# Optimization experiments

Measured on AMD Instinct MI355X. Metric: run time of the kernel, lower is better.

## Reference

```python
import jax, jax.numpy as jnp
import numpy as np
from jax import lax

B, N, CIN, COUT, FPS, K, TCH, M, H = 8, 4096, 128, 256, 1024, 24, 256, 32, 4
HD = TCH // H
BN_SCALE = 1.0 / np.sqrt(1.0 + 1e-5)  # eval-mode BN: running_mean=0, running_var=1


def _gather(points, idx):
    # points [B,N,C], idx [B,S] or [B,S,K] -> gathered points
    return jax.vmap(lambda p, i: p[i])(points, idx)


def _bn(x, g, b):
    return x * (g * BN_SCALE) + b


def _ln(x, g, b):
    mu = jnp.mean(x, -1, keepdims=True)
    v = jnp.var(x, -1, keepdims=True)
    return (x - mu) / jnp.sqrt(v + 1e-5) * g + b


def _gelu(x):
    return jax.nn.gelu(x, approximate=False)


def _fps(xyz, npoint, farthest0):
    Bb, Nn, _ = xyz.shape
    def step(carry, _):
        dmin, far = carry
        c = jax.vmap(lambda p, i: p[i])(xyz, far)  # [B,3]
        d = jnp.sum((xyz - c[:, None, :]) ** 2, -1)
        dmin = jnp.minimum(dmin, d)
        return (dmin, jnp.argmax(dmin, -1)), far
    init = (jnp.full((Bb, Nn), 1e10, xyz.dtype), farthest0)
    _, cents = lax.scan(step, init, None, length=npoint)
    return cents.T  # [B, npoint]


def _sqdist(src, dst):
    d = -2.0 * jnp.einsum('bnc,bmc->bnm', src, dst)
    d = d + jnp.sum(src ** 2, -1)[:, :, None]
    d = d + jnp.sum(dst ** 2, -1)[:, None, :]
    return d


def _forward(xyz, x, t, farthest0, Wproj, gproj, bproj, Wl1, gl1, bl1, Wl2, gl2, bl2,
             Wc1, gc1, bc1, Wc2, gc2, bc2, Wq, Wk, Wv, Wo,
             ln1g, ln1b, Wqkv, Wao, ln2g, ln2b, Wf1, Wf2):
    # --- GenerateGraph: FPS + KNN grouping ---
    fps_idx = _fps(xyz, FPS, farthest0)            # [B,S]
    new_xyz = _gather(xyz, fps_idx)                # [B,S,3]
    xT = jnp.transpose(x, (0, 2, 1))               # [B,N,Cin]
    new_pts = _gather(xT, fps_idx)                 # [B,S,Cin]
    dist = _sqdist(new_xyz, xyz)                   # [B,S,N]
    _, idx = lax.top_k(-dist, K)                   # [B,S,K] nearest neighbors
    grouped = _gather(xT, idx)                     # [B,S,K,Cin]
    edge = grouped - new_pts[:, :, None, :]
    # --- Local: Conv1DBR proj + Conv1DBRRes (channels-last, 1x1 convs = GEMM) ---
    h = _gelu(_bn(jnp.einsum('bskc,oc->bsko', edge, Wproj), gproj, bproj))
    r = _gelu(_bn(jnp.einsum('bsko,po->bskp', h, Wl1), gl1, bl1))
    r = _bn(jnp.einsum('bskp,op->bsko', r, Wl2), gl2, bl2)
    h = _gelu(r + h)
    f = jnp.max(h, axis=2)                         # adaptive_max_pool over k -> [B,S,O]
    # --- Channel (ca): Conv1DBRRes on centroid features ---
    r = _gelu(_bn(f @ Wc1.T, gc1, bc1))
    r = _bn(r @ Wc2.T, gc2, bc2)
    f = _gelu(r + f)
    x_out = jnp.transpose(f, (0, 2, 1))            # [B,O,S]
    # --- Local2Former: tokens attend to local features ---
    q = t @ Wq.T
    kk = f @ Wk.T
    v = f @ Wv.T
    a = jax.nn.softmax(jnp.einsum('bmd,bsd->bms', q, kk) * (TCH ** -0.5), axis=-1)
    t = t + jnp.einsum('bms,bsd->bmd', a, v) @ Wo.T
    # --- Former: one pre-norm encoder layer (MHA + MLP) ---
    hn = _ln(t, ln1g, ln1b)
    qkv = (hn @ Wqkv.T).reshape(B, M, 3, H, HD).transpose(2, 0, 3, 1, 4)
    qh, kh, vh = qkv[0], qkv[1], qkv[2]            # [B,H,M,hd]
    attn = jax.nn.softmax(jnp.einsum('bhmd,bhnd->bhmn', qh, kh) * (HD ** -0.5), axis=-1)
    o = jnp.einsum('bhmn,bhnd->bhmd', attn, vh).transpose(0, 2, 1, 3).reshape(B, M, TCH)
    t = t + o @ Wao.T
    hn = _ln(t, ln2g, ln2b)
    t = t + _gelu(hn @ Wf1.T) @ Wf2.T
    return new_xyz, x_out, t


def setup_inputs() -> dict:
    key = jax.random.key(0)
    ks = jax.random.split(key, 40)
    def w(k, o, i):
        return jax.random.normal(k, (o, i), jnp.float32) / np.sqrt(i)
    def g(k, c):
        return 1.0 + 0.1 * jax.random.normal(k, (c,), jnp.float32)
    def bta(k, c):
        return 0.1 * jax.random.normal(k, (c,), jnp.float32)
    inp = {
        'xyz': jax.random.normal(ks[0], (B, N, 3), jnp.float32),
        'x': jax.random.normal(ks[1], (B, CIN, N), jnp.float32),
        't': jax.random.normal(ks[2], (B, M, TCH), jnp.float32),
        'farthest0': jax.random.randint(ks[3], (B,), 0, N),
        'Wproj': w(ks[4], COUT, CIN), 'gproj': g(ks[5], COUT), 'bproj': bta(ks[6], COUT),
        'Wl1': w(ks[7], COUT, COUT), 'gl1': g(ks[8], COUT), 'bl1': bta(ks[9], COUT),
        'Wl2': w(ks[10], COUT, COUT), 'gl2': g(ks[11], COUT), 'bl2': bta(ks[12], COUT),
        'Wc1': w(ks[13], COUT, COUT), 'gc1': g(ks[14], COUT), 'bc1': bta(ks[15], COUT),
        'Wc2': w(ks[16], COUT, COUT), 'gc2': g(ks[17], COUT), 'bc2': bta(ks[18], COUT),
        'Wq': w(ks[19], TCH, TCH), 'Wk': w(ks[20], TCH, COUT), 'Wv': w(ks[21], TCH, COUT),
        'Wo': w(ks[22], TCH, TCH),
        'ln1g': g(ks[23], TCH), 'ln1b': bta(ks[24], TCH),
        'Wqkv': w(ks[25], 3 * TCH, TCH), 'Wao': w(ks[26], TCH, TCH),
        'ln2g': g(ks[27], TCH), 'ln2b': bta(ks[28], TCH),
        'Wf1': w(ks[29], 2 * TCH, TCH), 'Wf2': w(ks[30], TCH, 2 * TCH),
    }
    return inp


def reference(xyz, x, t, farthest0, Wproj, gproj, bproj, Wl1, gl1, bl1, Wl2, gl2, bl2,
              Wc1, gc1, bc1, Wc2, gc2, bc2, Wq, Wk, Wv, Wo,
              ln1g, ln1b, Wqkv, Wao, ln2g, ln2b, Wf1, Wf2):
    return _forward(xyz, x, t, farthest0, Wproj, gproj, bproj, Wl1, gl1, bl1, Wl2, gl2, bl2,
                    Wc1, gc1, bc1, Wc2, gc2, bc2, Wq, Wk, Wv, Wo,
                    ln1g, ln1b, Wqkv, Wao, ln2g, ln2b, Wf1, Wf2)
```

## Files before the change

### kernel.cpp

```cpp
#include <hip/hip_runtime.h>
#include <math.h>

#define Bc 8
#define Nc 4096
#define CINc 128
#define COUTc 256
#define Sc 1024
#define Kc 24
#define TCHc 256
#define Mc 32
#define Hc 4
#define HDc 64
#define MBAT (Sc*Kc)

#define BN_SCALE_F 0.9999950000374997f

typedef __attribute__((ext_vector_type(8))) short bf16x8;
typedef __attribute__((ext_vector_type(4))) float f32x4;

__device__ __forceinline__ float b2f(short s){
  unsigned int u = ((unsigned int)(unsigned short)s) << 16;
  union { unsigned int u; float f; } c; c.u = u; return c.f;
}
__device__ __forceinline__ short f2b(float f){
  union { unsigned int u; float f; } c; c.f = f;
  unsigned int u = c.u;
  unsigned int r = (u + 0x7fffu + ((u >> 16) & 1u)) >> 16;
  return (short)(r & 0xffffu);
}
__device__ __forceinline__ float gelu_f(float v){
  return 0.5f * v * (1.f + erff(v * 0.7071067811865475f));
}
__device__ __forceinline__ float rdval(const float* p){ return *p; }
__device__ __forceinline__ float rdval(const short* p){ return b2f(*p); }
__device__ __forceinline__ void wrval(float* p, float v){ *p = v; }
__device__ __forceinline__ void wrval(short* p, float v){ *p = f2b(v); }

__device__ __forceinline__ void gl_lds16(const short* g, short* l){
  __builtin_amdgcn_global_load_lds(
     (const __attribute__((address_space(1))) void*)g,
     (__attribute__((address_space(3))) void*)l, 16, 0, 0);
}

template<int CTRL>
__device__ __forceinline__ double dpp_max_f64(double v){
  long long x = __double_as_longlong(v);
  int lo = (int)(unsigned int)(x & 0xFFFFFFFFLL);
  int hi = (int)(unsigned int)((unsigned long long)x >> 32);
  int plo = __builtin_amdgcn_update_dpp(lo, lo, CTRL, 0xF, 0xF, false);
  int phi = __builtin_amdgcn_update_dpp(hi, hi, CTRL, 0xF, 0xF, false);
  double p = __longlong_as_double((long long)(((unsigned long long)(unsigned int)phi << 32)
                                              | (unsigned int)plo));
  return fmax(v, p);
}
template<int CTRL>
__device__ __forceinline__ float dpp_min_f32(float v){
  int x = __float_as_int(v);
  int p = __builtin_amdgcn_update_dpp(x, x, CTRL, 0xF, 0xF, false);
  return fminf(v, __int_as_float(p));
}
template<int CTRL>
__device__ __forceinline__ unsigned dpp_min_u32(unsigned v){
  int p = __builtin_amdgcn_update_dpp((int)v, (int)v, CTRL, 0xF, 0xF, false);
  unsigned pu = (unsigned)p;
  return v < pu ? v : pu;
}

#define PREP_FPS 8
#define PREP_TX 4096
#define PREP_CVT 64
#define PREP_DD 128
#define PREP_TOTAL (PREP_FPS+PREP_TX+PREP_CVT+PREP_DD)

__global__ __launch_bounds__(256) void prep_kernel(
    const float* __restrict__ xyz, const int* __restrict__ far0, int* __restrict__ fps_idx,
    const float* __restrict__ x, short* __restrict__ xT,
    const float* __restrict__ Wproj, const float* __restrict__ Wl1, const float* __restrict__ Wl2,
    const float* __restrict__ Wc1, const float* __restrict__ Wc2,
    const float* __restrict__ Wk, const float* __restrict__ Wv,
    const float* __restrict__ Wq, const float* __restrict__ Wo,
    const float* __restrict__ Wqkv, const float* __restrict__ Wao,
    const float* __restrict__ Wf1, const float* __restrict__ Wf2,
    const float* __restrict__ t_in,
    short* __restrict__ wbf, float* __restrict__ dd){
  __shared__ double smem[6176];
  int bid = blockIdx.x, tid = threadIdx.x;
  if(bid < PREP_FPS){
    int b = bid;
    float* sx = (float*)smem;
    float* sy = sx + Nc;
    float* sz = sy + Nc;
    double* pwave = smem + (Nc*12)/8;
    const float* xb = xyz + (size_t)b*Nc*3;
    for(int i=tid; i<Nc; i+=256){
      const float* p = xb + i*3;
      sx[i]=p[0]; sy[i]=p[1]; sz[i]=p[2];
    }
    __syncthreads();
    float px[16], py[16], pz[16], dmin[16];
    unsigned int lokey[16];
#pragma unroll
    for(int j=0;j<16;j++){
      int n = tid + 256*j;
      px[j]=sx[n]; py[j]=sy[n]; pz[j]=sz[n];
      dmin[j]=1e10f;
      lokey[j]=(unsigned int)((Nc-1) - n);
    }
    int winner = far0[b] & (Nc-1);
    int* out = fps_idx + b*Sc;
    for(int it=0; it<Sc; it++){
      if(tid==0) out[it] = winner;
      float cx=sx[winner], cy=sy[winner], cz=sz[winner];
      double key[16];
#pragma unroll
      for(int j=0;j<16;j++){
        float dx = __fsub_rn(px[j], cx);
        float dy = __fsub_rn(py[j], cy);
        float dz = __fsub_rn(pz[j], cz);
        float d = __fadd_rn(__fadd_rn(__fmul_rn(dx,dx), __fmul_rn(dy,dy)), __fmul_rn(dz,dz));
        dmin[j] = fminf(dmin[j], d);
        unsigned long long k = (((unsigned long long)__float_as_uint(dmin[j])) << 32) | lokey[j];
        key[j] = __longlong_as_double((long long)k);
      }
#pragma unroll
      for(int st=8; st>0; st>>=1)
#pragma unroll
        for(int j=0;j<st;j++) key[j] = fmax(key[j], key[j+st]);
      double kv = key[0];
      kv = dpp_max_f64<0x111>(kv);
      kv = dpp_max_f64<0x112>(kv);
      kv = dpp_max_f64<0x114>(kv);
      kv = dpp_max_f64<0x118>(kv);
      kv = dpp_max_f64<0x142>(kv);
      kv = dpp_max_f64<0x143>(kv);
      int p = it & 1;
      if((tid & 63) == 63) pwave[p*4 + (tid>>6)] = kv;
      __syncthreads();
      double k0 = pwave[p*4+0], k1 = pwave[p*4+1], k2 = pwave[p*4+2], k3 = pwave[p*4+3];
      double kb = fmax(fmax(k0,k1), fmax(k2,k3));
      unsigned long long kbits = (unsigned long long)__double_as_longlong(kb);
      winner = (Nc-1) - (int)(kbits & 0xFFFFFFFFULL);
    }
  } else if(bid < PREP_FPS+PREP_TX){
    int t = bid - PREP_FPS;
    int b = t >> 9;
    int rem = t & 511;
    int n0 = (rem & 127) * 32;
    int c0 = (rem >> 7) * 32;
    short (*tile)[33] = (short(*)[33])smem;
    int tx = tid & 31, ty = tid >> 5;
#pragma unroll
    for(int i=0;i<32;i+=8)
      tile[ty+i][tx] = f2b(x[((size_t)b*CINc + (c0+ty+i))*Nc + n0+tx]);
    __syncthreads();
#pragma unroll
    for(int i=0;i<32;i+=8)
      xT[((size_t)b*Nc + (n0+ty+i))*CINc + c0+tx] = tile[tx][ty+i];
  } else if(bid < PREP_FPS+PREP_TX+PREP_CVT){
    int gid = (bid - PREP_FPS - PREP_TX)*256 + tid;
    const int stride = PREP_CVT*256;
    short* p = wbf;
    for(int i=gid; i<COUTc*CINc; i+=stride) p[i] = f2b(Wproj[i]);
    p += COUTc*CINc;
    for(int i=gid; i<COUTc*COUTc; i+=stride) p[i] = f2b(Wl1[i]);
    p += COUTc*COUTc;
    for(int i=gid; i<COUTc*COUTc; i+=stride) p[i] = f2b(Wl2[i]);
    p += COUTc*COUTc;
    for(int i=gid; i<COUTc*COUTc; i+=stride) p[i] = f2b(Wc1[i]);
    p += COUTc*COUTc;
    for(int i=gid; i<COUTc*COUTc; i+=stride) p[i] = f2b(Wc2[i]);
    p += COUTc*COUTc;
    for(int i=gid; i<TCHc*COUTc; i+=stride) p[i] = f2b(Wk[i]);
    p += TCHc*COUTc;
    for(int i=gid; i<TCHc*COUTc; i+=stride) p[i] = f2b(Wv[i]);
    p += TCHc*COUTc;
    for(int i=gid; i<TCHc*TCHc; i+=stride) p[i] = f2b(Wq[i]);
    p += TCHc*TCHc;
    for(int i=gid; i<TCHc*TCHc; i+=stride) p[i] = f2b(Wo[i]);
    p += TCHc*TCHc;
    for(int i=gid; i<3*TCHc*TCHc; i+=stride) p[i] = f2b(Wqkv[i]);
    p += 3*TCHc*TCHc;
    for(int i=gid; i<TCHc*TCHc; i+=stride) p[i] = f2b(Wao[i]);
    p += TCHc*TCHc;
    for(int i=gid; i<2*TCHc*TCHc; i+=stride) p[i] = f2b(Wf1[i]);
    p += 2*TCHc*TCHc;
    for(int i=gid; i<2*TCHc*TCHc; i+=stride) p[i] = f2b(Wf2[i]);
    p += 2*TCHc*TCHc;
    for(int i=gid; i<Bc*Mc*TCHc; i+=stride) p[i] = f2b(t_in[i]);
  } else {
    int i = (bid - PREP_FPS - PREP_TX - PREP_CVT)*256 + tid;
    const float* p = xyz + (size_t)i*3;
    float xx=p[0], yy=p[1], zz=p[2];
    dd[i] = __fadd_rn(__fadd_rn(__fmul_rn(xx,xx),__fmul_rn(yy,yy)),__fmul_rn(zz,zz));
  }
}

__global__ __launch_bounds__(256) void knn_kernel(const float* __restrict__ xyz,
                                                  const int* __restrict__ fps_idx,
                                                  const float* __restrict__ dd,
                                                  int* __restrict__ knn_idx,
                                                  float* __restrict__ out0){
  int bs = blockIdx.x, tid = threadIdx.x;
  int b = bs >> 10;
  __shared__ float pv[4]; __shared__ int pi[4];
  int qn = fps_idx[bs] & (Nc-1);
  const float* q = xyz + ((size_t)b*Nc + qn)*3;
  float sx = q[0], sy = q[1], sz = q[2];
  if(tid < 3) out0[bs*3 + tid] = q[tid];
  float ss = __fadd_rn(__fadd_rn(__fmul_rn(sx,sx),__fmul_rn(sy,sy)),__fmul_rn(sz,sz));
  const float* xb = xyz + (size_t)b*Nc*3;
  const float* db = dd + b*Nc;
  float dv[16];
#pragma unroll
  for(int j=0;j<16;j++){
    int n = tid + 256*j;
    float xx=xb[n*3], yy=xb[n*3+1], zz=xb[n*3+2];
    float e = __fmul_rn(sx,xx);
    e = __fadd_rn(e, __fmul_rn(sy,yy));
    e = __fadd_rn(e, __fmul_rn(sz,zz));
    dv[j] = __fadd_rn(__fadd_rn(__fmul_rn(-2.f,e), ss), db[n]);
  }
  int* ob = knn_idx + (size_t)bs*Kc;
  for(int k=0;k<Kc;k++){
    float bvv = dv[0];
#pragma unroll
    for(int j=1;j<16;j++) bvv = fminf(bvv, dv[j]);
    bvv = dpp_min_f32<0x111>(bvv);
    bvv = dpp_min_f32<0x112>(bvv);
    bvv = dpp_min_f32<0x114>(bvv);
    bvv = dpp_min_f32<0x118>(bvv);
    bvv = dpp_min_f32<0x142>(bvv);
    bvv = dpp_min_f32<0x143>(bvv);
    if((tid&63)==63) pv[tid>>6] = bvv;
    __syncthreads();
    float vmin = fminf(fminf(pv[0],pv[1]), fminf(pv[2],pv[3]));
    unsigned bi = 0xFFFFFFFFu;
#pragma unroll
    for(int j=0;j<16;j++){
      unsigned n = (unsigned)(tid + 256*j);
      if(dv[j]==vmin && n < bi) bi = n;
    }
    bi = dpp_min_u32<0x111>(bi);
    bi = dpp_min_u32<0x112>(bi);
    bi = dpp_min_u32<0x114>(bi);
    bi = dpp_min_u32<0x118>(bi);
    bi = dpp_min_u32<0x142>(bi);
    bi = dpp_min_u32<0x143>(bi);
    if((tid&63)==63) pi[tid>>6] = (int)bi;
    __syncthreads();
    unsigned i0=(unsigned)pi[0], i1=(unsigned)pi[1], i2=(unsigned)pi[2], i3=(unsigned)pi[3];
    unsigned m01 = i0<i1?i0:i1, m23 = i2<i3?i2:i3;
    unsigned win = m01<m23?m01:m23;
    if(tid==0) ob[k] = (int)(win & (Nc-1));
#pragma unroll
    for(int j=0;j<16;j++) if((int)win == tid + 256*j) dv[j] = 3.4e38f;
  }
}

template<int HAS_BN, int HAS_GELU, int HAS_RES, typename TRES>
__global__ __launch_bounds__(256) void gemm128(
    const short* __restrict__ A, const short* __restrict__ W,
    const float* __restrict__ g, const float* __restrict__ bias,
    const TRES* __restrict__ Res, short* __restrict__ Out,
    int Nn, int Kk){
  __shared__ short As[128*32];
  __shared__ short Bs[128*32];
  int bm = blockIdx.y*128, bn = blockIdx.x*128;
  int tid = threadIdx.x;
  int wave = tid>>6, lane = tid&63, quad = lane>>4, l16 = lane&15;
  int wr = (wave>>1)*64, wc = (wave&1)*64;
  f32x4 acc[4][4];
#pragma unroll
  for(int i=0;i<4;i++)
#pragma unroll
    for(int j=0;j<4;j++) acc[i][j] = (f32x4){0.f,0.f,0.f,0.f};
  int sr = tid>>2, scc = (tid&3)*8;
  const short* Ap = A + (size_t)(bm+sr)*Kk + scc;
  const short* Wp = W + (size_t)(bn+sr)*Kk + scc;
  for(int k0=0; k0<Kk; k0+=32){
    gl_lds16(Ap + k0,                    As + tid*8);
    gl_lds16(Ap + k0 + (size_t)64*Kk,    As + 2048 + tid*8);
    gl_lds16(Wp + k0,                    Bs + tid*8);
    gl_lds16(Wp + k0 + (size_t)64*Kk,    Bs + 2048 + tid*8);
    __syncthreads();
    bf16x8 af[4], bfr[4];
#pragma unroll
    for(int mt=0; mt<4; mt++) af[mt]  = *(const bf16x8*)&As[(wr+mt*16+l16)*32 + quad*8];
#pragma unroll
    for(int nt=0; nt<4; nt++) bfr[nt] = *(const bf16x8*)&Bs[(wc+nt*16+l16)*32 + quad*8];
#pragma unroll
    for(int mt=0; mt<4; mt++)
#pragma unroll
      for(int nt=0; nt<4; nt++)
        acc[mt][nt] = __builtin_amdgcn_mfma_f32_16x16x32_bf16(af[mt], bfr[nt], acc[mt][nt], 0, 0, 0);
    __syncthreads();
  }
#pragma unroll
  for(int nt=0; nt<4; nt++){
    int col = bn + wc + nt*16 + l16;
    float gs = 0.f, bs_ = 0.f;
    if(HAS_BN){ gs = g[col] * BN_SCALE_F; bs_ = bias[col]; }
#pragma unroll
    for(int mt=0; mt<4; mt++){
#pragma unroll
      for(int r2=0;r2<4;r2++){
        int row = bm + wr + mt*16 + quad*4 + r2;
        float v = acc[mt][nt][r2];
        if(HAS_BN) v = v*gs + bs_;
        if(HAS_RES) v += rdval(Res + (size_t)row*Nn + col);
        if(HAS_GELU) v = gelu_f(v);
        Out[(size_t)row*Nn + col] = f2b(v);
      }
    }
  }
}

__global__ __launch_bounds__(256) void proj128(
    const short* __restrict__ xT, const int* __restrict__ knn_idx, const int* __restrict__ fps_idx,
    const short* __restrict__ W, const float* __restrict__ g, const float* __restrict__ bias,
    short* __restrict__ Out, int R0){
  __shared__ short As[128*32];
  __shared__ short Bs[128*32];
  int bm = blockIdx.y*128, bn = blockIdx.x*128;
  int tid = threadIdx.x;
  int wave = tid>>6, lane = tid&63, quad = lane>>4, l16 = lane&15;
  int wr = (wave>>1)*64, wc = (wave&1)*64;
  f32x4 acc[4][4];
#pragma unroll
  for(int i=0;i<4;i++)
#pragma unroll
    for(int j=0;j<4;j++) acc[i][j] = (f32x4){0.f,0.f,0.f,0.f};
  int sr = tid>>2, scc = (tid&3)*8;
  int Rg0 = R0 + bm + sr, Rg1 = Rg0 + 64;
  int b0 = Rg0 / (Sc*Kc), b1 = Rg1 / (Sc*Kc);
  int nk0 = knn_idx[Rg0] & (Nc-1), nk1 = knn_idx[Rg1] & (Nc-1);
  int nc0 = fps_idx[Rg0 / Kc] & (Nc-1), nc1 = fps_idx[Rg1 / Kc] & (Nc-1);
  const short* pk0 = xT + ((size_t)b0*Nc + nk0)*CINc + scc;
  const short* pc0 = xT + ((size_t)b0*Nc + nc0)*CINc + scc;
  const short* pk1 = xT + ((size_t)b1*Nc + nk1)*CINc + scc;
  const short* pc1 = xT + ((size_t)b1*Nc + nc1)*CINc + scc;
  const short* Wp  = W + (size_t)(bn+sr)*CINc + scc;
  for(int k0=0; k0<CINc; k0+=32){
    gl_lds16(Wp + k0,                      Bs + tid*8);
    gl_lds16(Wp + k0 + (size_t)64*CINc,    Bs + 2048 + tid*8);
    bf16x8 vk = *(const bf16x8*)(pk0 + k0);
    bf16x8 vc = *(const bf16x8*)(pc0 + k0);
    bf16x8 e0, e1;
#pragma unroll
    for(int i=0;i<8;i++) e0[i] = f2b(__fsub_rn(b2f(vk[i]), b2f(vc[i])));
    vk = *(const bf16x8*)(pk1 + k0);
    vc = *(const bf16x8*)(pc1 + k0);
#pragma unroll
    for(int i=0;i<8;i++) e1[i] = f2b(__fsub_rn(b2f(vk[i]), b2f(vc[i])));
    *(bf16x8*)&As[tid*8] = e0;
    *(bf16x8*)&As[2048 + tid*8] = e1;
    __syncthreads();
    bf16x8 af[4], bfr[4];
#pragma unroll
    for(int mt=0; mt<4; mt++) af[mt]  = *(const bf16x8*)&As[(wr+mt*16+l16)*32 + quad*8];
#pragma unroll
    for(int nt=0; nt<4; nt++) bfr[nt] = *(const bf16x8*)&Bs[(wc+nt*16+l16)*32 + quad*8];
#pragma unroll
    for(int mt=0; mt<4; mt++)
#pragma unroll
      for(int nt=0; nt<4; nt++)
        acc[mt][nt] = __builtin_amdgcn_mfma_f32_16x16x32_bf16(af[mt], bfr[nt], acc[mt][nt], 0, 0, 0);
    __syncthreads();
  }
#pragma unroll
  for(int nt=0; nt<4; nt++){
    int col = bn + wc + nt*16 + l16;
    float gs = g[col] * BN_SCALE_F, bs_ = bias[col];
#pragma unroll
    for(int mt=0; mt<4; mt++){
#pragma unroll
      for(int r2=0;r2<4;r2++){
        int row = bm + wr + mt*16 + quad*4 + r2;
        float v = acc[mt][nt][r2]*gs + bs_;
        Out[(size_t)row*COUTc + col] = f2b(gelu_f(v));
      }
    }
  }
}

__global__ __launch_bounds__(192) void gemm_l2max(
    const short* __restrict__ A, const short* __restrict__ W,
    const float* __restrict__ g, const float* __restrict__ bias,
    const short* __restrict__ Hres, short* __restrict__ Fout, int R0){
  __shared__ short As[48*32];
  __shared__ short Bs[64*32];
  __shared__ float sm[48][65];
  int bm = blockIdx.y*48, bn = blockIdx.x*64;
  int tid = threadIdx.x;
  int wave = tid >> 6, lane = tid & 63, quad = lane >> 4, l16 = lane & 15;
  f32x4 acc[4];
#pragma unroll
  for(int i=0;i<4;i++) acc[i] = (f32x4){0.f,0.f,0.f,0.f};
  const short* Ap  = A + (size_t)(bm + (tid>>2))*COUTc + (tid&3)*8;
  const short* Wp  = W + (size_t)(bn + (tid>>2))*COUTc + (tid&3)*8;
  const short* Wp2 = W + (size_t)(bn + 48 + (lane>>2))*COUTc + (lane&3)*8;
  for(int k0=0; k0<COUTc; k0+=32){
    gl_lds16(Ap + k0, As + tid*8);
    gl_lds16(Wp + k0, Bs + tid*8);
    if(wave==0) gl_lds16(Wp2 + k0, Bs + 1536 + lane*8);
    __syncthreads();
    bf16x8 a = *(const bf16x8*)&As[(wave*16 + l16)*32 + quad*8];
#pragma unroll
    for(int ct=0; ct<4; ct++){
      bf16x8 bb = *(const bf16x8*)&Bs[(ct*16 + l16)*32 + quad*8];
      acc[ct] = __builtin_amdgcn_mfma_f32_16x16x32_bf16(a, bb, acc[ct], 0, 0, 0);
    }
    __syncthreads();
  }
#pragma unroll
  for(int ct=0; ct<4; ct++){
    int col = bn + ct*16 + l16;
    float gs = g[col] * BN_SCALE_F, bs_ = bias[col];
#pragma unroll
    for(int r2=0;r2<4;r2++){
      int rl = wave*16 + quad*4 + r2;
      float v = acc[ct][r2]*gs + bs_;
      v += b2f(Hres[(size_t)(bm+rl)*COUTc + col]);
      sm[rl][ct*16 + l16] = gelu_f(v);
    }
  }
  __syncthreads();
  if(tid < 128){
    int gl = tid >> 6, col = tid & 63;
    float mx = -3.4e38f;
#pragma unroll
    for(int kk=0; kk<Kc; kk++) mx = fmaxf(mx, sm[gl*Kc + kk][col]);
    int gg = R0/Kc + blockIdx.y*2 + gl;
    Fout[(size_t)gg*COUTc + bn + col] = f2b(mx);
  }
}

template<int HAS_BN, int HAS_GELU, int HAS_RES, typename TRES, typename TOUT>
__global__ __launch_bounds__(256) void gemm64d(
    const short* __restrict__ A, const short* __restrict__ W,
    const float* __restrict__ g, const float* __restrict__ bias,
    const TRES* __restrict__ Res, TOUT* __restrict__ Out,
    int Nn, int Kk){
  __shared__ short As[64*32];
  __shared__ short Bs[64*32];
  int bm = blockIdx.y*64, bn = blockIdx.x*64;
  int tid = threadIdx.x;
  int wave = tid >> 6, lane = tid & 63, quad = lane >> 4, l16 = lane & 15;
  f32x4 acc[4];
#pragma unroll
  for(int i=0;i<4;i++) acc[i] = (f32x4){0.f,0.f,0.f,0.f};
  const short* Ap = A + (size_t)(bm + (tid>>2))*Kk + (tid&3)*8;
  const short* Wp = W + (size_t)(bn + (tid>>2))*Kk + (tid&3)*8;
  for(int k0=0; k0<Kk; k0+=32){
    gl_lds16(Ap + k0, As + tid*8);
    gl_lds16(Wp + k0, Bs + tid*8);
    __syncthreads();
    bf16x8 a = *(const bf16x8*)&As[(wave*16 + l16)*32 + quad*8];
#pragma unroll
    for(int ct=0; ct<4; ct++){
      bf16x8 bb = *(const bf16x8*)&Bs[(ct*16 + l16)*32 + quad*8];
      acc[ct] = __builtin_amdgcn_mfma_f32_16x16x32_bf16(a, bb, acc[ct], 0, 0, 0);
    }
    __syncthreads();
  }
#pragma unroll
  for(int ct=0; ct<4; ct++){
    int col = bn + ct*16 + l16;
    float gs = 0.f, bs_ = 0.f;
    if(HAS_BN){ gs = g[col] * BN_SCALE_F; bs_ = bias[col]; }
#pragma unroll
    for(int r2=0;r2<4;r2++){
      int row = bm + wave*16 + quad*4 + r2;
      float v = acc[ct][r2];
      if(HAS_BN) v = v*gs + bs_;
      if(HAS_RES) v += rdval(Res + (size_t)row*Nn + col);
      if(HAS_GELU) v = gelu_f(v);
      wrval(Out + (size_t)row*Nn + col, v);
    }
  }
}

__global__ __launch_bounds__(256) void transpose_f(const short* __restrict__ f2, float* __restrict__ out1){
  __shared__ short tile[32][33];
  int b = blockIdx.z;
  int s0 = blockIdx.x*32, c0 = blockIdx.y*32;
  int tx = threadIdx.x & 31, ty = threadIdx.x >> 5;
#pragma unroll
  for(int i=0;i<32;i+=8)
    tile[ty+i][tx] = f2[((size_t)b*Sc + (s0+ty+i))*COUTc + c0+tx];
  __syncthreads();
#pragma unroll
  for(int i=0;i<32;i+=8)
    out1[((size_t)b*COUTc + (c0+ty+i))*Sc + s0+tx] = b2f(tile[tx][ty+i]);
}

__global__ __launch_bounds__(256) void l2f_attn(
    const short* __restrict__ qb, const short* __restrict__ kv,
    short* __restrict__ ao){
  int blk = blockIdx.x; int b = blk / Mc; int m = blk % Mc;
  int tid = threadIdx.x;
  __shared__ float qs[TCHc];
  __shared__ float aw[Sc];
  __shared__ float red[8];
  qs[tid] = b2f(qb[(size_t)(b*Mc+m)*TCHc + tid]);
  __syncthreads();
  float sc[4];
#pragma unroll
  for(int jj=0;jj<4;jj++){
    int j = tid + 256*jj;
    const short* kp = kv + ((size_t)b*Sc + j)*512;
    float a = 0.f;
    for(int c=0;c<TCHc;c+=8){
      bf16x8 v8 = *(const bf16x8*)(kp + c);
#pragma unroll
      for(int i=0;i<8;i++) a += b2f(v8[i]) * qs[c+i];
    }
    sc[jj] = a * 0.0625f;
  }
  float mx = fmaxf(fmaxf(sc[0],sc[1]), fmaxf(sc[2],sc[3]));
#pragma unroll
  for(int off=32; off>0; off>>=1) mx = fmaxf(mx, __shfl_xor(mx, off));
  if((tid&63)==0) red[tid>>6] = mx;
  __syncthreads();
  mx = fmaxf(fmaxf(red[0],red[1]), fmaxf(red[2],red[3]));
  float se = 0.f;
#pragma unroll
  for(int jj=0;jj<4;jj++){
    float e = expf(sc[jj] - mx);
    aw[tid + 256*jj] = e;
    se += e;
  }
#pragma unroll
  for(int off=32; off>0; off>>=1) se += __shfl_xor(se, off);
  if((tid&63)==0) red[4 + (tid>>6)] = se;
  __syncthreads();
  se = red[4]+red[5]+red[6]+red[7];
  float inv = 1.f/se;
#pragma unroll
  for(int jj=0;jj<4;jj++) aw[tid + 256*jj] *= inv;
  __syncthreads();
  float acc = 0.f;
  const short* vp = kv + (size_t)b*Sc*512 + 256 + tid;
  for(int j=0;j<Sc;j++) acc += aw[j] * b2f(vp[(size_t)j*512]);
  ao[(size_t)(b*Mc+m)*TCHc + tid] = f2b(acc);
}

__global__ __launch_bounds__(64) void former_attn(const short* __restrict__ qkv, short* __restrict__ oa){
  int blk = blockIdx.x;
  int m = blk % Mc; int bh = blk / Mc; int h = bh % Hc; int b = bh / Hc;
  int lane = threadIdx.x;
  __shared__ float qs[HDc];
  __shared__ float aw2[32];
  const short* base = qkv + (size_t)(b*Mc)*(3*TCHc);
  qs[lane] = b2f(base[(size_t)m*3*TCHc + h*HDc + lane]);
  __syncthreads();
  int j = lane & 31;
  const short* kp = base + (size_t)j*3*TCHc + TCHc + h*HDc;
  float s = 0.f;
  for(int d=0; d<HDc; d+=8){
    bf16x8 v8 = *(const bf16x8*)(kp + d);
#pragma unroll
    for(int i=0;i<8;i++) s += b2f(v8[i]) * qs[d+i];
  }
  s *= 0.125f;
  float mx = s;
#pragma unroll
  for(int off=16; off>0; off>>=1) mx = fmaxf(mx, __shfl_xor(mx, off, 32));
  float e = expf(s - mx);
  float se = e;
#pragma unroll
  for(int off=16; off>0; off>>=1) se += __shfl_xor(se, off, 32);
  if(lane < 32) aw2[lane] = e / se;
  __syncthreads();
  float acc = 0.f;
  const short* vp = base + 2*TCHc + h*HDc + lane;
  for(int jj=0; jj<32; jj++) acc += aw2[jj] * b2f(vp[(size_t)jj*3*TCHc]);
  oa[(size_t)(b*Mc+m)*TCHc + h*HDc + lane] = f2b(acc);
}

__global__ __launch_bounds__(64) void ln_kernel(const float* __restrict__ X, const float* __restrict__ g,
                                                const float* __restrict__ bb, short* __restrict__ O){
  int row = blockIdx.x, lane = threadIdx.x;
  const float* xp = X + (size_t)row*TCHc;
  float x[4];
#pragma unroll
  for(int j2=0;j2<4;j2++) x[j2] = xp[lane + 64*j2];
  float sm = x[0]+x[1]+x[2]+x[3];
#pragma unroll
  for(int off=32; off>0; off>>=1) sm += __shfl_xor(sm, off);
  float mu = sm * (1.f/256.f);
  float vs = 0.f;
#pragma unroll
  for(int j2=0;j2<4;j2++){ float d = x[j2]-mu; vs += d*d; }
#pragma unroll
  for(int off=32; off>0; off>>=1) vs += __shfl_xor(vs, off);
  float var = vs * (1.f/256.f);
  float rstd = 1.f / sqrtf(var + 1e-5f);
#pragma unroll
  for(int j2=0;j2<4;j2++){
    int c = lane + 64*j2;
    float o = (x[j2]-mu)*rstd*g[c] + bb[c];
    O[(size_t)row*TCHc + c] = f2b(o);
  }
}

extern "C" void kernel_launch(void* const* d_in, const int* in_sizes, int n_in,
                              void* d_out, int out_size, void* d_ws, size_t ws_size,
                              hipStream_t stream){
  const float* xyz  = (const float*)d_in[0];
  const float* x    = (const float*)d_in[1];
  const float* t_in = (const float*)d_in[2];
  const int*   far0 = (const int*)d_in[3];
  const float* Wproj=(const float*)d_in[4];  const float* gproj=(const float*)d_in[5];  const float* bproj=(const float*)d_in[6];
  const float* Wl1 = (const float*)d_in[7];  const float* gl1 = (const float*)d_in[8];  const float* bl1 = (const float*)d_in[9];
  const float* Wl2 = (const float*)d_in[10]; const float* gl2 = (const float*)d_in[11]; const float* bl2 = (const float*)d_in[12];
  const float* Wc1 = (const float*)d_in[13]; const float* gc1 = (const float*)d_in[14]; const float* bc1 = (const float*)d_in[15];
  const float* Wc2 = (const float*)d_in[16]; const float* gc2 = (const float*)d_in[17]; const float* bc2 = (const float*)d_in[18];
  const float* Wq  = (const float*)d_in[19]; const float* Wk  = (const float*)d_in[20]; const float* Wv  = (const float*)d_in[21];
  const float* Wo  = (const float*)d_in[22];
  const float* ln1g= (const float*)d_in[23]; const float* ln1b= (const float*)d_in[24];
  const float* Wqkv= (const float*)d_in[25]; const float* Wao = (const float*)d_in[26];
  const float* ln2g= (const float*)d_in[27]; const float* ln2b= (const float*)d_in[28];
  const float* Wf1 = (const float*)d_in[29]; const float* Wf2 = (const float*)d_in[30];

  char* wsb = (char*)d_ws;
  size_t off = 0;
  auto alloc = [&](size_t bytes)->void*{ void* p = wsb + off; off += (bytes + 255) & ~(size_t)255; return p; };
  int*   fps_i = (int*)alloc((size_t)Bc*Sc*4);
  float* ddb   = (float*)alloc((size_t)Bc*Nc*4);
  int*   knn   = (int*)alloc((size_t)Bc*Sc*Kc*4);
  short* xT    = (short*)alloc((size_t)Bc*Nc*CINc*2);
  size_t wbf_elems = (size_t)COUTc*CINc + 4*(size_t)COUTc*COUTc + 2*(size_t)TCHc*COUTc
                   + 2*(size_t)TCHc*TCHc + 3*(size_t)TCHc*TCHc + (size_t)TCHc*TCHc
                   + 2*(size_t)TCHc*TCHc + 2*(size_t)TCHc*TCHc + (size_t)Bc*Mc*TCHc;
  short* wbf   = (short*)alloc(wbf_elems*2);
  short* fbuf  = (short*)alloc((size_t)Bc*Sc*COUTc*2);
  short* rcbuf = (short*)alloc((size_t)Bc*Sc*COUTc*2);
  short* f2buf = (short*)alloc((size_t)Bc*Sc*COUTc*2);
  short* kvbuf = (short*)alloc((size_t)Bc*Sc*512*2);
  short* qbuf  = (short*)alloc((size_t)Bc*Mc*TCHc*2);
  short* a1out = (short*)alloc((size_t)Bc*Mc*TCHc*2);
  float* t1buf = (float*)alloc((size_t)Bc*Mc*TCHc*4);
  short* hnbuf = (short*)alloc((size_t)Bc*Mc*TCHc*2);
  short* qkvb  = (short*)alloc((size_t)Bc*Mc*3*TCHc*2);
  short* a2out = (short*)alloc((size_t)Bc*Mc*TCHc*2);
  float* t2buf = (float*)alloc((size_t)Bc*Mc*TCHc*4);
  short* hn2buf= (short*)alloc((size_t)Bc*Mc*TCHc*2);
  short* g1buf = (short*)alloc((size_t)Bc*Mc*2*TCHc*2);
  size_t full_bytes  = (size_t)Bc*MBAT*COUTc*2;
  size_t batch_bytes = (size_t)MBAT*COUTc*2;
  bool batched = (off + 2*(full_bytes + 256) <= ws_size);
  short* hbuf = (short*)alloc(batched ? full_bytes : batch_bytes);
  short* rbuf = (short*)alloc(batched ? full_bytes : batch_bytes);
  if(off > ws_size) return;

  short* wproj_bf = wbf;
  short* wl1_bf   = wproj_bf + COUTc*CINc;
  short* wl2_bf   = wl1_bf + COUTc*COUTc;
  short* wc1_bf   = wl2_bf + COUTc*COUTc;
  short* wc2_bf   = wc1_bf + COUTc*COUTc;
  short* wkv_bf   = wc2_bf + COUTc*COUTc;
  short* wq_bf    = wkv_bf + 2*TCHc*COUTc;
  short* wo_bf    = wq_bf + TCHc*TCHc;
  short* wqkv_bf  = wo_bf + TCHc*TCHc;
  short* wao_bf   = wqkv_bf + 3*TCHc*TCHc;
  short* wf1_bf   = wao_bf + TCHc*TCHc;
  short* wf2_bf   = wf1_bf + 2*TCHc*TCHc;
  short* tbf      = wf2_bf + 2*TCHc*TCHc;

  float* out0 = (float*)d_out;
  float* out1 = out0 + (size_t)Bc*Sc*3;
  float* out2 = out1 + (size_t)Bc*COUTc*Sc;

  prep_kernel<<<PREP_TOTAL, 256, 0, stream>>>(xyz, far0, fps_i, x, xT,
                                              Wproj, Wl1, Wl2, Wc1, Wc2, Wk, Wv,
                                              Wq, Wo, Wqkv, Wao, Wf1, Wf2, t_in, wbf, ddb);
  knn_kernel<<<Bc*Sc, 256, 0, stream>>>(xyz, fps_i, ddb, knn, out0);
  if(batched){
    proj128<<<dim3(COUTc/128, (Bc*MBAT)/128), 256, 0, stream>>>(xT, knn, fps_i, wproj_bf, gproj, bproj, hbuf, 0);
    gemm128<1,1,0,short><<<dim3(COUTc/128, (Bc*MBAT)/128), 256, 0, stream>>>(hbuf, wl1_bf, gl1, bl1, (const short*)nullptr, rbuf, COUTc, COUTc);
    gemm_l2max<<<dim3(COUTc/64, (Bc*MBAT)/48), 192, 0, stream>>>(rbuf, wl2_bf, gl2, bl2, hbuf, fbuf, 0);
  } else {
    for(int b=0; b<Bc; b++){
      proj128<<<dim3(COUTc/128, MBAT/128), 256, 0, stream>>>(xT, knn, fps_i, wproj_bf, gproj, bproj, hbuf, b*MBAT);
      gemm128<1,1,0,short><<<dim3(COUTc/128, MBAT/128), 256, 0, stream>>>(hbuf, wl1_bf, gl1, bl1, (const short*)nullptr, rbuf, COUTc, COUTc);
      gemm_l2max<<<dim3(COUTc/64, MBAT/48), 192, 0, stream>>>(rbuf, wl2_bf, gl2, bl2, hbuf, fbuf, b*MBAT);
    }
  }
  gemm64d<1,1,0,short,short><<<dim3(COUTc/64, (Bc*Sc)/64), 256, 0, stream>>>(fbuf, wc1_bf, gc1, bc1, (const short*)nullptr, rcbuf, COUTc, COUTc);
  gemm64d<1,1,1,short,short><<<dim3(COUTc/64, (Bc*Sc)/64), 256, 0, stream>>>(rcbuf, wc2_bf, gc2, bc2, fbuf, f2buf, COUTc, COUTc);
  transpose_f<<<dim3(Sc/32, COUTc/32, Bc), 256, 0, stream>>>(f2buf, out1);
  gemm64d<0,0,0,short,short><<<dim3(TCHc/64, (Bc*Mc)/64), 256, 0, stream>>>(tbf, wq_bf, nullptr, nullptr, (const short*)nullptr, qbuf, TCHc, TCHc);
  gemm64d<0,0,0,short,short><<<dim3(512/64, (Bc*Sc)/64), 256, 0, stream>>>(f2buf, wkv_bf, nullptr, nullptr, (const short*)nullptr, kvbuf, 512, COUTc);
  l2f_attn<<<Bc*Mc, 256, 0, stream>>>(qbuf, kvbuf, a1out);
  gemm64d<0,0,1,float,float><<<dim3(TCHc/64, (Bc*Mc)/64), 256, 0, stream>>>(a1out, wo_bf, nullptr, nullptr, t_in, t1buf, TCHc, TCHc);
  ln_kernel<<<Bc*Mc, 64, 0, stream>>>(t1buf, ln1g, ln1b, hnbuf);
  gemm64d<0,0,0,short,short><<<dim3((3*TCHc)/64, (Bc*Mc)/64), 256, 0, stream>>>(hnbuf, wqkv_bf, nullptr, nullptr, (const short*)nullptr, qkvb, 3*TCHc, TCHc);
  former_attn<<<Bc*Hc*Mc, 64, 0, stream>>>(qkvb, a2out);
  gemm64d<0,0,1,float,float><<<dim3(TCHc/64, (Bc*Mc)/64), 256, 0, stream>>>(a2out, wao_bf, nullptr, nullptr, t1buf, t2buf, TCHc, TCHc);
  ln_kernel<<<Bc*Mc, 64, 0, stream>>>(t2buf, ln2g, ln2b, hn2buf);
  gemm64d<0,1,0,short,short><<<dim3((2*TCHc)/64, (Bc*Mc)/64), 256, 0, stream>>>(hn2buf, wf1_bf, nullptr, nullptr, (const short*)nullptr, g1buf, 2*TCHc, TCHc);
  gemm64d<0,0,1,float,float><<<dim3(TCHc/64, (Bc*Mc)/64), 256, 0, stream>>>(g1buf, wf2_bf, nullptr, nullptr, t2buf, out2, TCHc, 2*TCHc);
}
```

Baseline: 1.211 ms.

## Fuse KNN into prep kernel and overlap it with FPS via progress flags

The separate KNN launch is removed, and KNN now runs inside the prep kernel as a persistent grid of 248 worker blocks, 31 per batch. FPS blocks publish centroid indices and a release-ordered progress counter every 8 iterations. Workers spin on that counter, so neighbour search for early centroids overlaps the serial FPS loop instead of waiting for it to finish. The transpose and weight conversion are folded into the same worker blocks, and point coordinates and squared norms are kept in registers. The risks are deadlock if the 256 blocks are not all co-resident, spin-wait overhead, and less parallelism for KNN (248 blocks instead of 8192).

```diff
diff --git a/kernel.cpp b/kernel.cpp
--- a/kernel.cpp
+++ b/kernel.cpp
@@ -67,10 +67,8 @@
 }
 
 #define PREP_FPS 8
-#define PREP_TX 4096
-#define PREP_CVT 64
-#define PREP_DD 128
-#define PREP_TOTAL (PREP_FPS+PREP_TX+PREP_CVT+PREP_DD)
+#define PREP_TOTAL 256
+#define NWORK 248
 
 __global__ __launch_bounds__(256) void prep_kernel(
     const float* __restrict__ xyz, const int* __restrict__ far0, int* __restrict__ fps_idx,
@@ -82,7 +80,8 @@
     const float* __restrict__ Wqkv, const float* __restrict__ Wao,
     const float* __restrict__ Wf1, const float* __restrict__ Wf2,
     const float* __restrict__ t_in,
-    short* __restrict__ wbf, float* __restrict__ dd){
+    short* __restrict__ wbf, int* __restrict__ prog,
+    int* __restrict__ knn_idx, float* __restrict__ out0){
   __shared__ double smem[6176];
   int bid = blockIdx.x, tid = threadIdx.x;
   if(bid < PREP_FPS){
@@ -109,7 +108,11 @@
     int winner = far0[b] & (Nc-1);
     int* out = fps_idx + b*Sc;
     for(int it=0; it<Sc; it++){
-      if(tid==0) out[it] = winner;
+      if(tid==0){
+        __hip_atomic_store(&out[it], winner, __ATOMIC_RELAXED, __HIP_MEMORY_SCOPE_AGENT);
+        if((it & 7) == 7)
+          __hip_atomic_store(&prog[b], it+1, __ATOMIC_RELEASE, __HIP_MEMORY_SCOPE_AGENT);
+      }
       float cx=sx[winner], cy=sy[winner], cz=sz[winner];
       double key[16];
 #pragma unroll
@@ -141,119 +144,128 @@
       unsigned long long kbits = (unsigned long long)__double_as_longlong(kb);
       winner = (Nc-1) - (int)(kbits & 0xFFFFFFFFULL);
     }
-  } else if(bid < PREP_FPS+PREP_TX){
-    int t = bid - PREP_FPS;
-    int b = t >> 9;
-    int rem = t & 511;
-    int n0 = (rem & 127) * 32;
-    int c0 = (rem >> 7) * 32;
+  } else {
+    int wid = bid - PREP_FPS;
+    int b = wid / 31;
+    int widb = wid % 31;
     short (*tile)[33] = (short(*)[33])smem;
-    int tx = tid & 31, ty = tid >> 5;
-#pragma unroll
-    for(int i=0;i<32;i+=8)
-      tile[ty+i][tx] = f2b(x[((size_t)b*CINc + (c0+ty+i))*Nc + n0+tx]);
-    __syncthreads();
-#pragma unroll
-    for(int i=0;i<32;i+=8)
-      xT[((size_t)b*Nc + (n0+ty+i))*CINc + c0+tx] = tile[tx][ty+i];
-  } else if(bid < PREP_FPS+PREP_TX+PREP_CVT){
-    int gid = (bid - PREP_FPS - PREP_TX)*256 + tid;
-    const int stride = PREP_CVT*256;
-    short* p = wbf;
-    for(int i=gid; i<COUTc*CINc; i+=stride) p[i] = f2b(Wproj[i]);
-    p += COUTc*CINc;
-    for(int i=gid; i<COUTc*COUTc; i+=stride) p[i] = f2b(Wl1[i]);
-    p += COUTc*COUTc;
-    for(int i=gid; i<COUTc*COUTc; i+=stride) p[i] = f2b(Wl2[i]);
-    p += COUTc*COUTc;
-    for(int i=gid; i<COUTc*COUTc; i+=stride) p[i] = f2b(Wc1[i]);
-    p += COUTc*COUTc;
-    for(int i=gid; i<COUTc*COUTc; i+=stride) p[i] = f2b(Wc2[i]);
-    p += COUTc*COUTc;
-    for(int i=gid; i<TCHc*COUTc; i+=stride) p[i] = f2b(Wk[i]);
-    p += TCHc*COUTc;
-    for(int i=gid; i<TCHc*COUTc; i+=stride) p[i] = f2b(Wv[i]);
-    p += TCHc*COUTc;
-    for(int i=gid; i<TCHc*TCHc; i+=stride) p[i] = f2b(Wq[i]);
-    p += TCHc*TCHc;
-    for(int i=gid; i<TCHc*TCHc; i+=stride) p[i] = f2b(Wo[i]);
-    p += TCHc*TCHc;
-    for(int i=gid; i<3*TCHc*TCHc; i+=stride) p[i] = f2b(Wqkv[i]);
-    p += 3*TCHc*TCHc;
-    for(int i=gid; i<TCHc*TCHc; i+=stride) p[i] = f2b(Wao[i]);
-    p += TCHc*TCHc;
-    for(int i=gid; i<2*TCHc*TCHc; i+=stride) p[i] = f2b(Wf1[i]);
-    p += 2*TCHc*TCHc;
-    for(int i=gid; i<2*TCHc*TCHc; i+=stride) p[i] = f2b(Wf2[i]);
-    p += 2*TCHc*TCHc;
-    for(int i=gid; i<Bc*Mc*TCHc; i+=stride) p[i] = f2b(t_in[i]);
-  } else {
-    int i = (bid - PREP_FPS - PREP_TX - PREP_CVT)*256 + tid;
-    const float* p = xyz + (size_t)i*3;
-    float xx=p[0], yy=p[1], zz=p[2];
-    dd[i] = __fadd_rn(__fadd_rn(__fmul_rn(xx,xx),__fmul_rn(yy,yy)),__fmul_rn(zz,zz));
-  }
-}
-
-__global__ __launch_bounds__(256) void knn_kernel(const float* __restrict__ xyz,
-                                                  const int* __restrict__ fps_idx,
-                                                  const float* __restrict__ dd,
-                                                  int* __restrict__ knn_idx,
-                                                  float* __restrict__ out0){
-  int bs = blockIdx.x, tid = threadIdx.x;
-  int b = bs >> 10;
-  __shared__ float pv[4]; __shared__ int pi[4];
-  int qn = fps_idx[bs] & (Nc-1);
-  const float* q = xyz + ((size_t)b*Nc + qn)*3;
-  float sx = q[0], sy = q[1], sz = q[2];
-  if(tid < 3) out0[bs*3 + tid] = q[tid];
-  float ss = __fadd_rn(__fadd_rn(__fmul_rn(sx,sx),__fmul_rn(sy,sy)),__fmul_rn(sz,sz));
-  const float* xb = xyz + (size_t)b*Nc*3;
-  const float* db = dd + b*Nc;
-  float dv[16];
-#pragma unroll
-  for(int j=0;j<16;j++){
-    int n = tid + 256*j;
-    float xx=xb[n*3], yy=xb[n*3+1], zz=xb[n*3+2];
-    float e = __fmul_rn(sx,xx);
-    e = __fadd_rn(e, __fmul_rn(sy,yy));
-    e = __fadd_rn(e, __fmul_rn(sz,zz));
-    dv[j] = __fadd_rn(__fadd_rn(__fmul_rn(-2.f,e), ss), db[n]);
-  }
-  int* ob = knn_idx + (size_t)bs*Kc;
-  for(int k=0;k<Kc;k++){
-    float bvv = dv[0];
-#pragma unroll
-    for(int j=1;j<16;j++) bvv = fminf(bvv, dv[j]);
-    bvv = dpp_min_f32<0x111>(bvv);
-    bvv = dpp_min_f32<0x112>(bvv);
-    bvv = dpp_min_f32<0x114>(bvv);
-    bvv = dpp_min_f32<0x118>(bvv);
-    bvv = dpp_min_f32<0x142>(bvv);
-    bvv = dpp_min_f32<0x143>(bvv);
-    if((tid&63)==63) pv[tid>>6] = bvv;
-    __syncthreads();
-    float vmin = fminf(fminf(pv[0],pv[1]), fminf(pv[2],pv[3]));
-    unsigned bi = 0xFFFFFFFFu;
+    for(int t = wid; t < 4096; t += NWORK){
+      int bb = t >> 9;
+      int rem = t & 511;
+      int n0 = (rem & 127) * 32;
+      int c0 = (rem >> 7) * 32;
+      int tx = tid & 31, ty = tid >> 5;
+      __syncthreads();
+#pragma unroll
+      for(int i=0;i<32;i+=8)
+        tile[ty+i][tx] = f2b(x[((size_t)bb*CINc + (c0+ty+i))*Nc + n0+tx]);
+      __syncthreads();
+#pragma unroll
+      for(int i=0;i<32;i+=8)
+        xT[((size_t)bb*Nc + (n0+ty+i))*CINc + c0+tx] = tile[tx][ty+i];
+    }
+    {
+      int gid = wid*256 + tid;
+      const int stride = NWORK*256;
+      short* p = wbf;
+      for(int i=gid; i<COUTc*CINc; i+=stride) p[i] = f2b(Wproj[i]);
+      p += COUTc*CINc;
+      for(int i=gid; i<COUTc*COUTc; i+=stride) p[i] = f2b(Wl1[i]);
+      p += COUTc*COUTc;
+      for(int i=gid; i<COUTc*COUTc; i+=stride) p[i] = f2b(Wl2[i]);
+      p += COUTc*COUTc;
+      for(int i=gid; i<COUTc*COUTc; i+=stride) p[i] = f2b(Wc1[i]);
+      p += COUTc*COUTc;
+      for(int i=gid; i<COUTc*COUTc; i+=stride) p[i] = f2b(Wc2[i]);
+      p += COUTc*COUTc;
+      for(int i=gid; i<TCHc*COUTc; i+=stride) p[i] = f2b(Wk[i]);
+      p += TCHc*COUTc;
+      for(int i=gid; i<TCHc*COUTc; i+=stride) p[i] = f2b(Wv[i]);
+      p += TCHc*COUTc;
+      for(int i=gid; i<TCHc*TCHc; i+=stride) p[i] = f2b(Wq[i]);
+      p += TCHc*TCHc;
+      for(int i=gid; i<TCHc*TCHc; i+=stride) p[i] = f2b(Wo[i]);
+      p += TCHc*TCHc;
+      for(int i=gid; i<3*TCHc*TCHc; i+=stride) p[i] = f2b(Wqkv[i]);
+      p += 3*TCHc*TCHc;
+      for(int i=gid; i<TCHc*TCHc; i+=stride) p[i] = f2b(Wao[i]);
+      p += TCHc*TCHc;
+      for(int i=gid; i<2*TCHc*TCHc; i+=stride) p[i] = f2b(Wf1[i]);
+      p += 2*TCHc*TCHc;
+      for(int i=gid; i<2*TCHc*TCHc; i+=stride) p[i] = f2b(Wf2[i]);
+      p += 2*TCHc*TCHc;
+      for(int i=gid; i<Bc*Mc*TCHc; i+=stride) p[i] = f2b(t_in[i]);
+    }
+    int* s_qn = (int*)smem;
+    float* pv = (float*)smem + 4;
+    int*   pi = (int*)smem + 8;
+    const float* xb = xyz + (size_t)b*Nc*3;
+    float px[16], py[16], pz[16], db[16];
 #pragma unroll
     for(int j=0;j<16;j++){
-      unsigned n = (unsigned)(tid + 256*j);
-      if(dv[j]==vmin && n < bi) bi = n;
-    }
-    bi = dpp_min_u32<0x111>(bi);
-    bi = dpp_min_u32<0x112>(bi);
-    bi = dpp_min_u32<0x114>(bi);
-    bi = dpp_min_u32<0x118>(bi);
-    bi = dpp_min_u32<0x142>(bi);
-    bi = dpp_min_u32<0x143>(bi);
-    if((tid&63)==63) pi[tid>>6] = (int)bi;
-    __syncthreads();
-    unsigned i0=(unsigned)pi[0], i1=(unsigned)pi[1], i2=(unsigned)pi[2], i3=(unsigned)pi[3];
-    unsigned m01 = i0<i1?i0:i1, m23 = i2<i3?i2:i3;
-    unsigned win = m01<m23?m01:m23;
-    if(tid==0) ob[k] = (int)(win & (Nc-1));
-#pragma unroll
-    for(int j=0;j<16;j++) if((int)win == tid + 256*j) dv[j] = 3.4e38f;
+      int n = tid + 256*j;
+      float xx=xb[n*3], yy=xb[n*3+1], zz=xb[n*3+2];
+      px[j]=xx; py[j]=yy; pz[j]=zz;
+      db[j] = __fadd_rn(__fadd_rn(__fmul_rn(xx,xx),__fmul_rn(yy,yy)),__fmul_rn(zz,zz));
+    }
+    __syncthreads();
+    for(int s = widb; s < Sc; s += 31){
+      if(tid==0){
+        while((unsigned)__hip_atomic_load(&prog[b], __ATOMIC_ACQUIRE, __HIP_MEMORY_SCOPE_AGENT) <= (unsigned)s)
+          __builtin_amdgcn_s_sleep(8);
+        int qn = __hip_atomic_load(&fps_idx[b*Sc + s], __ATOMIC_RELAXED, __HIP_MEMORY_SCOPE_AGENT) & (Nc-1);
+        s_qn[0] = qn;
+      }
+      __syncthreads();
+      int qn = s_qn[0];
+      const float* q = xyz + ((size_t)b*Nc + qn)*3;
+      float sx = q[0], sy = q[1], sz = q[2];
+      if(tid < 3) out0[((size_t)b*Sc + s)*3 + tid] = q[tid];
+      float ss = __fadd_rn(__fadd_rn(__fmul_rn(sx,sx),__fmul_rn(sy,sy)),__fmul_rn(sz,sz));
+      float dv[16];
+#pragma unroll
+      for(int j=0;j<16;j++){
+        float e = __fmul_rn(sx,px[j]);
+        e = __fadd_rn(e, __fmul_rn(sy,py[j]));
+        e = __fadd_rn(e, __fmul_rn(sz,pz[j]));
+        dv[j] = __fadd_rn(__fadd_rn(__fmul_rn(-2.f,e), ss), db[j]);
+      }
+      int* ob = knn_idx + ((size_t)b*Sc + s)*Kc;
+      for(int k=0;k<Kc;k++){
+        float bvv = dv[0];
+#pragma unroll
+        for(int j=1;j<16;j++) bvv = fminf(bvv, dv[j]);
+        bvv = dpp_min_f32<0x111>(bvv);
+        bvv = dpp_min_f32<0x112>(bvv);
+        bvv = dpp_min_f32<0x114>(bvv);
+        bvv = dpp_min_f32<0x118>(bvv);
+        bvv = dpp_min_f32<0x142>(bvv);
+        bvv = dpp_min_f32<0x143>(bvv);
+        if((tid&63)==63) pv[tid>>6] = bvv;
+        __syncthreads();
+        float vmin = fminf(fminf(pv[0],pv[1]), fminf(pv[2],pv[3]));
+        unsigned bi = 0xFFFFFFFFu;
+#pragma unroll
+        for(int j=0;j<16;j++){
+          unsigned n = (unsigned)(tid + 256*j);
+          if(dv[j]==vmin && n < bi) bi = n;
+        }
+        bi = dpp_min_u32<0x111>(bi);
+        bi = dpp_min_u32<0x112>(bi);
+        bi = dpp_min_u32<0x114>(bi);
+        bi = dpp_min_u32<0x118>(bi);
+        bi = dpp_min_u32<0x142>(bi);
+        bi = dpp_min_u32<0x143>(bi);
+        if((tid&63)==63) pi[tid>>6] = (int)bi;
+        __syncthreads();
+        unsigned i0=(unsigned)pi[0], i1=(unsigned)pi[1], i2=(unsigned)pi[2], i3=(unsigned)pi[3];
+        unsigned m01 = i0<i1?i0:i1, m23 = i2<i3?i2:i3;
+        unsigned win = m01<m23?m01:m23;
+        if(tid==0) ob[k] = (int)(win & (Nc-1));
+#pragma unroll
+        for(int j=0;j<16;j++) if((int)win == tid + 256*j) dv[j] = 3.4e38f;
+      }
+    }
   }
 }
 
@@ -626,8 +638,8 @@
   char* wsb = (char*)d_ws;
   size_t off = 0;
   auto alloc = [&](size_t bytes)->void*{ void* p = wsb + off; off += (bytes + 255) & ~(size_t)255; return p; };
+  int*   prog  = (int*)alloc(Bc*4);
   int*   fps_i = (int*)alloc((size_t)Bc*Sc*4);
-  float* ddb   = (float*)alloc((size_t)Bc*Nc*4);
   int*   knn   = (int*)alloc((size_t)Bc*Sc*Kc*4);
   short* xT    = (short*)alloc((size_t)Bc*Nc*CINc*2);
   size_t wbf_elems = (size_t)COUTc*CINc + 4*(size_t)COUTc*COUTc + 2*(size_t)TCHc*COUTc
@@ -672,10 +684,11 @@
   float* out1 = out0 + (size_t)Bc*Sc*3;
   float* out2 = out1 + (size_t)Bc*COUTc*Sc;
 
+  hipMemsetAsync(prog, 0, Bc*4, stream);
   prep_kernel<<<PREP_TOTAL, 256, 0, stream>>>(xyz, far0, fps_i, x, xT,
                                               Wproj, Wl1, Wl2, Wc1, Wc2, Wk, Wv,
-                                              Wq, Wo, Wqkv, Wao, Wf1, Wf2, t_in, wbf, ddb);
-  knn_kernel<<<Bc*Sc, 256, 0, stream>>>(xyz, fps_i, ddb, knn, out0);
+                                              Wq, Wo, Wqkv, Wao, Wf1, Wf2, t_in,
+                                              wbf, prog, knn, out0);
   if(batched){
     proj128<<<dim3(COUTc/128, (Bc*MBAT)/128), 256, 0, stream>>>(xT, knn, fps_i, wproj_bf, gproj, bproj, hbuf, 0);
     gemm128<1,1,0,short><<<dim3(COUTc/128, (Bc*MBAT)/128), 256, 0, stream>>>(hbuf, wl1_bf, gl1, bl1, (const short*)nullptr, rbuf, COUTc, COUTc);
```

After: 1.185 ms. -2.2%, faster.
